# Kernel tuning notes

Hardware: AMD Instinct MI355X
Metric: run time of the kernel (lower is better)

The kernel has to match this reference:

```python
import jax, jax.numpy as jnp
import numpy as np

G = 8          # grid_size
N = G * G      # 64 nodes
DEG = 17       # neighbors per node for 8x8 sudoku (2x4 boxes)
STEPS = 32
H = 96         # hidden_dim
E = 16         # embed_size
B = 16         # batch


def sudoku_edges():
    # row (7) + col (7) + 2x4 box (7) neighbors, set-union -> 17 per node
    idx = np.arange(N).reshape(G, G)
    nb = []
    for j in range(N):
        r, c = j // G, j % G
        br, bc = (r // 2) * 2, (c // 4) * 4
        s = set(idx[r, :].tolist()) | set(idx[:, c].tolist()) | set(idx[br:br + 2, bc:bc + 4].flatten().tolist())
        s.discard(j)
        nb.append(sorted(s))
    return np.asarray(nb, dtype=np.int32)  # [64, 17]


def setup_inputs() -> dict:
    key = jax.random.key(0)
    ks = jax.random.split(key, 16)
    sc = 0.05
    inp = {
        "x": jax.random.randint(ks[0], (B, G, G), 0, G + 1),            # given digits, 0 = blank
        "target": jax.random.randint(ks[1], (B, G, G), 0, G) + 1,       # solutions in 1..8
        "edges": jnp.asarray(sudoku_edges()),                            # [64, 17] int32
        "digit_emb": jax.random.normal(ks[2], (G + 1, E), jnp.float32) * sc,
        "row_emb": jax.random.normal(ks[3], (G, E), jnp.float32) * sc,
        "col_emb": jax.random.normal(ks[4], (G, E), jnp.float32) * sc,
        "in0_W": jax.random.normal(ks[5], (3 * E, H), jnp.float32) * sc,
        "in0_b": jnp.zeros((H,), jnp.float32),
        "in_Ws": jax.random.normal(ks[6], (3, H, H), jnp.float32) * sc,
        "in_bs": jnp.zeros((3, H), jnp.float32),
        "msg0_W": jax.random.normal(ks[7], (2 * H, H), jnp.float32) * sc,
        "msg0_b": jnp.zeros((H,), jnp.float32),
        "msg_Ws": jax.random.normal(ks[8], (3, H, H), jnp.float32) * sc,
        "msg_bs": jnp.zeros((3, H), jnp.float32),
        "W_ih": jax.random.normal(ks[9], (2 * H, 4 * H), jnp.float32) * sc,
        "W_hh": jax.random.normal(ks[10], (H, 4 * H), jnp.float32) * sc,
        "b_ih": jnp.zeros((4 * H,), jnp.float32),
        "b_hh": jnp.zeros((4 * H,), jnp.float32),
        "pred_W": jax.random.normal(ks[11], (H, G), jnp.float32) * sc,
        "pred_b": jnp.zeros((G,), jnp.float32),
    }
    return inp


def _mlp(z, W0, b0, Ws, bs):
    # Linear -> ReLU -> Linear -> ReLU -> Linear -> ReLU -> Linear (def_MLP)
    z = jax.nn.relu(z @ W0 + b0)
    z = jax.nn.relu(z @ Ws[0] + bs[0])
    z = jax.nn.relu(z @ Ws[1] + bs[1])
    return z @ Ws[2] + bs[2]


def reference(x, target, edges, digit_emb, row_emb, col_emb,
              in0_W, in0_b, in_Ws, in_bs,
              msg0_W, msg0_b, msg_Ws, msg_bs,
              W_ih, W_hh, b_ih, b_hh, pred_W, pred_b):
    bsz = x.shape[0]
    xf = x.reshape(bsz, N)
    tgt = target.reshape(bsz, N) - 1                      # labels 0..7

    de = digit_emb[xf]                                    # [B,64,E]
    re = row_emb[jnp.repeat(jnp.arange(G), G)]            # [64,E]
    ce = col_emb[jnp.tile(jnp.arange(G), G)]              # [64,E]
    feat = jnp.concatenate([de,
                            jnp.broadcast_to(re[None], (bsz, N, E)),
                            jnp.broadcast_to(ce[None], (bsz, N, E))], axis=-1)
    xin = _mlp(feat, in0_W, in0_b, in_Ws, in_bs)          # [B,64,H]

    h0 = jnp.zeros((bsz, N, H), jnp.float32)
    s0 = jnp.zeros((bsz * N, H), jnp.float32)

    def step(carry, _):
        h, s, loss = carry
        # gather-by-edge message passing
        h_edges = h[:, edges]                                             # [B,64,17,H]
        h_self = jnp.broadcast_to(h[:, :, None, :], (bsz, N, DEG, H))
        msg = _mlp(jnp.concatenate([h_edges, h_self], -1),
                   msg0_W, msg0_b, msg_Ws, msg_bs).sum(axis=2)            # [B,64,H]
        # LSTMCell update
        lstm_in = jnp.concatenate([msg, xin], -1).reshape(bsz * N, 2 * H)
        gates = lstm_in @ W_ih + b_ih + h.reshape(bsz * N, H) @ W_hh + b_hh
        i, f, g, o = jnp.split(gates, 4, axis=-1)
        s2 = jax.nn.sigmoid(f) * s + jax.nn.sigmoid(i) * jnp.tanh(g)
        h2 = (jax.nn.sigmoid(o) * jnp.tanh(s2)).reshape(bsz, N, H)
        # per-step prediction / loss / accuracy
        logp = jax.nn.log_softmax(h2 @ pred_W + pred_b, axis=-1)          # [B,64,8]
        pred = jnp.argmax(logp, axis=-1)
        acc = jnp.mean(jnp.all(pred == tgt, axis=1).astype(jnp.float32))
        loss_n = -jnp.sum(jnp.take_along_axis(logp, tgt[..., None], -1)) / (bsz * N)
        return (h2, s2, loss + loss_n), acc

    (h, s, loss), accs = jax.lax.scan(step, (h0, s0, jnp.float32(0.0)), None, length=STEPS)
    loss = loss / STEPS
    final_pred = jnp.argmax(h @ pred_W + pred_b, axis=-1)                 # [B,64]
    return loss, accs, final_pred
```

## Files before the change

kernel.cpp:

```cpp
#include <hip/hip_runtime.h>

#define DEG 17
#define NSTEPS 32
#define HD 96
#define NODES 1024

#define WS_U0     0
#define WS_BAR    196608
#define WS_U1     196864
#define WS_XIN    393472
#define WS_GX     491776
#define WS_LOSSP  884992
#define WS_CNTP   893184

#define Z1    0
#define Z2    7680
#define P3    0
#define PL    0
#define PU    0
#define W1L   15360
#define W2L   24576
#define GXL   33792
#define GATES 35328
#define MSGH  36864
#define S3T   37632
#define H2T   38016
#define SLC   38400
#define MSGB  38784
#define M0B   39072
#define LGT   39168
#define NBRI  39200
#define SMTOT 39280

__global__ void init_kernel(
    const int* __restrict__ x,
    const float* __restrict__ digit_emb,
    const float* __restrict__ row_emb,
    const float* __restrict__ col_emb,
    const float* __restrict__ in0_W,
    const float* __restrict__ in0_b,
    const float* __restrict__ in_Ws,
    const float* __restrict__ in_bs,
    const float* __restrict__ msg0_b,
    float* __restrict__ xin,
    float* __restrict__ u0)
{
  const int node = blockIdx.x;
  const int j = threadIdx.x;
  const int n = node & 63;
  const int r = n >> 3, c = n & 7;
  __shared__ float feat[48];
  __shared__ float za[HD];
  __shared__ float zb[HD];
  if (j < 16)      feat[j] = digit_emb[x[node]*16 + j];
  else if (j < 32) feat[j] = row_emb[r*16 + (j-16)];
  else if (j < 48) feat[j] = col_emb[c*16 + (j-32)];
  u0[node*192 + 96 + j] = msg0_b[j];
  __syncthreads();
  float a = in0_b[j];
  for (int k = 0; k < 48; ++k) a = fmaf(feat[k], in0_W[k*HD + j], a);
  za[j] = fmaxf(a, 0.f);
  __syncthreads();
  a = in_bs[j];
  for (int k = 0; k < HD; ++k) a = fmaf(za[k], in_Ws[k*HD + j], a);
  zb[j] = fmaxf(a, 0.f);
  __syncthreads();
  a = in_bs[HD + j];
  for (int k = 0; k < HD; ++k) a = fmaf(zb[k], in_Ws[9216 + k*HD + j], a);
  za[j] = fmaxf(a, 0.f);
  __syncthreads();
  a = in_bs[2*HD + j];
  for (int k = 0; k < HD; ++k) a = fmaf(za[k], in_Ws[2*9216 + k*HD + j], a);
  xin[node*HD + j] = a;
}

__global__ __launch_bounds__(384) void gx_kernel(
    const float* __restrict__ xin, const float* __restrict__ W_ih,
    const float* __restrict__ b_ih, const float* __restrict__ b_hh,
    float* __restrict__ gx)
{
  __shared__ float xs[4*HD];
  const int tid = threadIdx.x;
  const int base = blockIdx.x * 4;
  {
    const int m = tid / HD, k = tid - m*HD;
    xs[m*HD + k] = xin[(base+m)*HD + k];
  }
  __syncthreads();
  const int j = tid;
  float a0 = b_ih[j] + b_hh[j], a1 = a0, a2 = a0, a3 = a0;
  for (int k = 0; k < HD; ++k) {
    const float w = W_ih[(96+k)*384 + j];
    a0 = fmaf(xs[k], w, a0);
    a1 = fmaf(xs[HD+k], w, a1);
    a2 = fmaf(xs[2*HD+k], w, a2);
    a3 = fmaf(xs[3*HD+k], w, a3);
  }
  gx[(base+0)*384 + j] = a0;
  gx[(base+1)*384 + j] = a1;
  gx[(base+2)*384 + j] = a2;
  gx[(base+3)*384 + j] = a3;
}

__global__ __launch_bounds__(512, 1) void solve_kernel(
    const int* __restrict__ edges,
    const float* __restrict__ msg0_W, const float* __restrict__ msg0_b,
    const float* __restrict__ msg_Ws, const float* __restrict__ msg_bs,
    const float* __restrict__ W_ih, const float* __restrict__ W_hh,
    const float* __restrict__ pred_W, const float* __restrict__ pred_b,
    const int* __restrict__ target,
    const float* __restrict__ gx,
    float* __restrict__ u0, float* __restrict__ u1,
    int* bar,
    float* __restrict__ lossP, int* __restrict__ cntP,
    float* __restrict__ final_pred_out)
{
  __shared__ float sm[SMTOT];

  const int tid = threadIdx.x;
  const int blk = blockIdx.x;
  const int bb = blk & 15;
  const int grp = blk >> 4;
  const int nbase = grp * 4;
  const int base = bb*64 + nbase;

  for (int i = tid*4; i < 9216; i += 2048) {
    *(float4*)&sm[W1L + i] = *(const float4*)&msg_Ws[i];
    *(float4*)&sm[W2L + i] = *(const float4*)&msg_Ws[9216 + i];
  }
  #pragma unroll
  for (int t = 0; t < 3; ++t) {
    const int idx = t*512 + tid;
    sm[GXL + idx] = gx[base*384 + idx];
  }
  if (tid < 288) sm[MSGB + tid] = msg_bs[tid];
  if (tid < 96)  sm[M0B + tid]  = msg0_b[tid];
  if (tid < 80) {
    const int m = tid / 20, r = tid % 20;
    ((int*)&sm[NBRI])[tid] = (r < DEG) ? (bb*64 + edges[(nbase+m)*DEG + r])*192 : -1;
  }
  if (tid < 384) {
    sm[SLC + tid] = 0.f;
    sm[MSGH + 384 + tid] = 0.f;
  }
  __syncthreads();

  const float* uP = u0;
  float*       uN = u1;

  for (int st = 0; st < NSTEPS; ++st) {
    if (tid < 480) {
      const int row = tid % 80;
      const int kh  = tid / 80;
      const int m = row / 20;
      const int k0 = kh * 16;
      const int nb = ((const int*)&sm[NBRI])[row];
      if (nb >= 0) {
        const float* ue = uP + nb + k0;
        const float* us = uP + (base+m)*192 + 96 + k0;
        #pragma unroll
        for (int t = 0; t < 4; ++t) {
          const float4 a = *(const float4*)(ue + 4*t);
          const float4 b = *(const float4*)(us + 4*t);
          sm[Z1 + (k0+4*t+0)*80 + row] = fmaxf(a.x + b.x, 0.f);
          sm[Z1 + (k0+4*t+1)*80 + row] = fmaxf(a.y + b.y, 0.f);
          sm[Z1 + (k0+4*t+2)*80 + row] = fmaxf(a.z + b.z, 0.f);
          sm[Z1 + (k0+4*t+3)*80 + row] = fmaxf(a.w + b.w, 0.f);
        }
      } else {
        #pragma unroll
        for (int t = 0; t < 16; ++t) sm[Z1 + (k0+t)*80 + row] = 0.f;
      }
    } else {
      const int i = tid - 480;
      #pragma unroll
      for (int t = 0; t < 12; ++t) sm[S3T + t*32 + i] = 0.f;
    }
    __syncthreads();

    if (tid < 480) {
      const int jg = tid % 24, dg = tid / 24;
      const int j4 = jg*4, d4 = dg*4;
      float acc[4][4] = {{0.f}};
      #pragma unroll 4
      for (int k = 0; k < 96; ++k) {
        const float4 z = *(const float4*)&sm[Z1 + k*80 + d4];
        const float4 w = *(const float4*)&sm[W1L + k*96 + j4];
        const float ze[4] = {z.x, z.y, z.z, z.w};
        const float we[4] = {w.x, w.y, w.z, w.w};
        #pragma unroll
        for (int dd = 0; dd < 4; ++dd)
          #pragma unroll
          for (int jj = 0; jj < 4; ++jj)
            acc[dd][jj] = fmaf(ze[dd], we[jj], acc[dd][jj]);
      }
      #pragma unroll
      for (int jj = 0; jj < 4; ++jj) {
        const float b1 = sm[MSGB + j4 + jj];
        float4 q;
        q.x = fmaxf(acc[0][jj] + b1, 0.f);
        q.y = fmaxf(acc[1][jj] + b1, 0.f);
        q.z = fmaxf(acc[2][jj] + b1, 0.f);
        q.w = fmaxf(acc[3][jj] + b1, 0.f);
        *(float4*)&sm[Z2 + (j4+jj)*80 + d4] = q;
      }
    }
    __syncthreads();

    if (tid < 480) {
      const int jg = tid % 24, dg = tid / 24;
      const int j4 = jg*4, d4 = dg*4;
      float acc[4][4] = {{0.f}};
      #pragma unroll 4
      for (int k = 0; k < 96; ++k) {
        const float4 z = *(const float4*)&sm[Z2 + k*80 + d4];
        const float4 w = *(const float4*)&sm[W2L + k*96 + j4];
        const float ze[4] = {z.x, z.y, z.z, z.w};
        const float we[4] = {w.x, w.y, w.z, w.w};
        #pragma unroll
        for (int dd = 0; dd < 4; ++dd)
          #pragma unroll
          for (int jj = 0; jj < 4; ++jj)
            acc[dd][jj] = fmaf(ze[dd], we[jj], acc[dd][jj]);
      }
      const int nd = d4 / 20;
      const int r0 = d4 - nd*20;
      #pragma unroll
      for (int jj = 0; jj < 4; ++jj) {
        const float b2 = sm[MSGB + 96 + j4 + jj];
        float p = 0.f;
        #pragma unroll
        for (int dd = 0; dd < 4; ++dd)
          if (r0 + dd < DEG) p += fmaxf(acc[dd][jj] + b2, 0.f);
        atomicAdd(&sm[S3T + (j4+jj)*4 + nd], p);
      }
    }
    __syncthreads();

    if (tid < 384) {
      const int jg = tid % 24, kq = tid / 24;
      const int j4 = jg*4, k0 = kq*6;
      const float* W3 = msg_Ws + 2*9216;
      float acc[4][4] = {{0.f}};
      #pragma unroll
      for (int kk = 0; kk < 6; ++kk) {
        const int k = k0 + kk;
        const float4 sv = *(const float4*)&sm[S3T + k*4];
        const float4 wv = *(const float4*)&W3[k*96 + j4];
        const float se[4] = {sv.x, sv.y, sv.z, sv.w};
        const float we[4] = {wv.x, wv.y, wv.z, wv.w};
        #pragma unroll
        for (int m = 0; m < 4; ++m)
          #pragma unroll
          for (int jj = 0; jj < 4; ++jj)
            acc[m][jj] = fmaf(se[m], we[jj], acc[m][jj]);
      }
      #pragma unroll
      for (int m = 0; m < 4; ++m) {
        float4 q = {acc[m][0], acc[m][1], acc[m][2], acc[m][3]};
        *(float4*)&sm[P3 + (kq*4 + m)*96 + j4] = q;
      }
    }
    __syncthreads();
    if (tid < 384) {
      const int m = tid / 96, j = tid % 96;
      float v = 17.f * sm[MSGB + 192 + j];
      #pragma unroll
      for (int kq = 0; kq < 16; ++kq) v += sm[P3 + (kq*4 + m)*96 + j];
      sm[MSGH + j*4 + m] = v;
    }
    __syncthreads();

    {
      const int jg = tid & 63, kq = tid >> 6;
      const int j6 = jg*6, k0 = kq*24;
      const float* Wb = (k0 < 96) ? (W_ih + (size_t)k0*384) : (W_hh + (size_t)(k0-96)*384);
      float acc[4][6] = {{0.f}};
      #pragma unroll 4
      for (int kk = 0; kk < 24; ++kk) {
        const float4 iv = *(const float4*)&sm[MSGH + (k0+kk)*4];
        const float* wp = Wb + kk*384 + j6;
        const float2 wa = *(const float2*)wp;
        const float2 wb2 = *(const float2*)(wp + 2);
        const float2 wc = *(const float2*)(wp + 4);
        const float ie[4] = {iv.x, iv.y, iv.z, iv.w};
        const float we[6] = {wa.x, wa.y, wb2.x, wb2.y, wc.x, wc.y};
        #pragma unroll
        for (int m = 0; m < 4; ++m)
          #pragma unroll
          for (int jj = 0; jj < 6; ++jj)
            acc[m][jj] = fmaf(ie[m], we[jj], acc[m][jj]);
      }
      #pragma unroll
      for (int m = 0; m < 4; ++m) {
        float2 qa = {acc[m][0], acc[m][1]};
        float2 qb = {acc[m][2], acc[m][3]};
        float2 qc = {acc[m][4], acc[m][5]};
        *(float2*)&sm[PL + (kq*4 + m)*384 + j6]     = qa;
        *(float2*)&sm[PL + (kq*4 + m)*384 + j6 + 2] = qb;
        *(float2*)&sm[PL + (kq*4 + m)*384 + j6 + 4] = qc;
      }
    }
    __syncthreads();
    {
      #pragma unroll
      for (int t = 0; t < 3; ++t) {
        const int idx = t*512 + tid;
        const int m = idx / 384, j = idx - m*384;
        float gv = sm[GXL + idx];
        #pragma unroll
        for (int kq = 0; kq < 8; ++kq) gv += sm[PL + (kq*4 + m)*384 + j];
        sm[GATES + idx] = gv;
      }
    }
    __syncthreads();

    if (tid < 384) {
      const int m = tid / 96, hj = tid - m*96;
      const float gi = sm[GATES + m*384 + hj];
      const float gf = sm[GATES + m*384 + 96 + hj];
      const float gg = sm[GATES + m*384 + 192 + hj];
      const float go = sm[GATES + m*384 + 288 + hj];
      const float sv = sm[SLC + tid];
      const float ig = 1.f/(1.f + expf(-gi));
      const float fg = 1.f/(1.f + expf(-gf));
      const float cg = tanhf(gg);
      const float og = 1.f/(1.f + expf(-go));
      const float s2 = fg*sv + ig*cg;
      const float h2 = og*tanhf(s2);
      sm[SLC + tid] = s2;
      sm[H2T + hj*4 + m] = h2;
      sm[MSGH + (96+hj)*4 + m] = h2;
    }
    __syncthreads();

    {
      const int jg = tid & 31, kq = tid >> 5;
      const int j6 = jg*6, k0 = kq*6;
      const float* Wb = (j6 < 96) ? (msg0_W + j6) : (msg0_W + 9216 + j6 - 96);
      float acc[4][6] = {{0.f}};
      #pragma unroll
      for (int kk = 0; kk < 6; ++kk) {
        const int k = k0 + kk;
        const float4 iv = *(const float4*)&sm[H2T + k*4];
        const float* wp = Wb + k*96;
        const float2 wa = *(const float2*)wp;
        const float2 wb2 = *(const float2*)(wp + 2);
        const float2 wc = *(const float2*)(wp + 4);
        const float ie[4] = {iv.x, iv.y, iv.z, iv.w};
        const float we[6] = {wa.x, wa.y, wb2.x, wb2.y, wc.x, wc.y};
        #pragma unroll
        for (int m = 0; m < 4; ++m)
          #pragma unroll
          for (int jj = 0; jj < 6; ++jj)
            acc[m][jj] = fmaf(ie[m], we[jj], acc[m][jj]);
      }
      #pragma unroll
      for (int m = 0; m < 4; ++m) {
        float2 qa = {acc[m][0], acc[m][1]};
        float2 qb = {acc[m][2], acc[m][3]};
        float2 qc = {acc[m][4], acc[m][5]};
        *(float2*)&sm[PU + (kq*4 + m)*192 + j6]     = qa;
        *(float2*)&sm[PU + (kq*4 + m)*192 + j6 + 2] = qb;
        *(float2*)&sm[PU + (kq*4 + m)*192 + j6 + 4] = qc;
      }
    }
    __syncthreads();
    {
      #pragma unroll
      for (int t = 0; t < 2; ++t) {
        const int idx = t*512 + tid;
        if (idx < 768) {
          const int m = idx / 192, j = idx - m*192;
          float v = (j >= 96) ? sm[M0B + j - 96] : 0.f;
          #pragma unroll
          for (int kq = 0; kq < 16; ++kq) v += sm[PU + (kq*4 + m)*192 + j];
          uN[(base+m)*192 + j] = v;
        }
      }
      if (tid >= 384) {
        const int t2 = tid - 384;
        const int m = t2 >> 5, c = (t2 >> 2) & 7, kq2 = t2 & 3;
        float p = 0.f;
        #pragma unroll
        for (int kk = 0; kk < 24; ++kk) {
          const int k = kq2*24 + kk;
          p = fmaf(sm[H2T + k*4 + m], pred_W[k*8 + c], p);
        }
        p += __shfl_xor(p, 1);
        p += __shfl_xor(p, 2);
        if (kq2 == 0) sm[LGT + m*8 + c] = p + pred_b[c];
      }
    }
    __syncthreads();

    if (tid < 4) {
      const int m = tid;
      const int node = base + m;
      float mx = sm[LGT + m*8];
      int pred = 0;
      #pragma unroll
      for (int c = 1; c < 8; ++c) {
        const float v = sm[LGT + m*8 + c];
        if (v > mx) { mx = v; pred = c; }
      }
      float sum = 0.f;
      #pragma unroll
      for (int c = 0; c < 8; ++c) sum += expf(sm[LGT + m*8 + c] - mx);
      const float lse = mx + logf(sum);
      const int tgt = target[node] - 1;
      sm[LGT + 16 + m] = lse - sm[LGT + m*8 + tgt];
      sm[LGT + 20 + m] = (pred == tgt) ? 1.f : 0.f;
      if (st == NSTEPS-1) final_pred_out[node] = (float)pred;
      if (m == 0) {
        lossP[st*256 + blk] = sm[LGT+16] + sm[LGT+17] + sm[LGT+18] + sm[LGT+19];
        cntP[st*256 + blk] = (int)(sm[LGT+20] + sm[LGT+21] + sm[LGT+22] + sm[LGT+23]);
      }
    }

    if (st < NSTEPS-1) {
      __syncthreads();
      if (tid == 0) {
        __hip_atomic_fetch_add(&bar[bb*16], 1, __ATOMIC_RELEASE, __HIP_MEMORY_SCOPE_AGENT);
        const int want = 16*(st+1);
        while (__hip_atomic_load(&bar[bb*16], __ATOMIC_RELAXED, __HIP_MEMORY_SCOPE_AGENT) < want)
          __builtin_amdgcn_s_sleep(2);
        __threadfence();
      }
      __syncthreads();
      float* tp = (float*)uP; uP = uN; uN = tp;
    }
  }
}

__global__ void finalize_kernel(const float* __restrict__ lossP,
                                const int* __restrict__ cntP,
                                float* __restrict__ out)
{
  __shared__ float sl[32];
  const int tid = threadIdx.x;
  const int st = tid >> 3, q = tid & 7;
  float lsum = 0.f;
  for (int i = 0; i < 32; ++i) lsum += lossP[st*256 + q*32 + i];
  lsum += __shfl_xor(lsum, 1);
  lsum += __shfl_xor(lsum, 2);
  lsum += __shfl_xor(lsum, 4);
  if (q == 0) sl[st] = lsum;
  float okc = 0.f;
  #pragma unroll
  for (int t = 0; t < 2; ++t) {
    const int bbat = q + 8*t;
    int c = 0;
    for (int i = 0; i < 16; ++i) c += cntP[st*256 + i*16 + bbat];
    okc += (c == 64) ? 1.f : 0.f;
  }
  okc += __shfl_xor(okc, 1);
  okc += __shfl_xor(okc, 2);
  okc += __shfl_xor(okc, 4);
  if (q == 0) out[1 + st] = okc / 16.f;
  __syncthreads();
  if (tid == 0) {
    float tot = 0.f;
    for (int i = 0; i < 32; ++i) tot += sl[i];
    out[0] = tot / ((float)NODES * (float)NSTEPS);
  }
}

extern "C" void kernel_launch(void* const* d_in, const int* in_sizes, int n_in,
                              void* d_out, int out_size, void* d_ws, size_t ws_size,
                              hipStream_t stream) {
  const int*   x         = (const int*)  d_in[0];
  const int*   target    = (const int*)  d_in[1];
  const int*   edges     = (const int*)  d_in[2];
  const float* digit_emb = (const float*)d_in[3];
  const float* row_emb   = (const float*)d_in[4];
  const float* col_emb   = (const float*)d_in[5];
  const float* in0_W     = (const float*)d_in[6];
  const float* in0_b     = (const float*)d_in[7];
  const float* in_Ws     = (const float*)d_in[8];
  const float* in_bs     = (const float*)d_in[9];
  const float* msg0_W    = (const float*)d_in[10];
  const float* msg0_b    = (const float*)d_in[11];
  const float* msg_Ws    = (const float*)d_in[12];
  const float* msg_bs    = (const float*)d_in[13];
  const float* W_ih      = (const float*)d_in[14];
  const float* W_hh      = (const float*)d_in[15];
  const float* b_ih      = (const float*)d_in[16];
  const float* b_hh      = (const float*)d_in[17];
  const float* pred_W    = (const float*)d_in[18];
  const float* pred_b    = (const float*)d_in[19];

  float* ws    = (float*)d_ws;
  float* u0    = ws + WS_U0;
  int*   bar   = (int*)(ws + WS_BAR);
  float* u1    = ws + WS_U1;
  float* xin   = ws + WS_XIN;
  float* gxb   = ws + WS_GX;
  float* lossP = ws + WS_LOSSP;
  int*   cntP  = (int*)(ws + WS_CNTP);

  hipMemsetAsync(d_ws, 0, (size_t)(196608 + 256)*sizeof(float), stream);

  init_kernel<<<NODES, HD, 0, stream>>>(x, digit_emb, row_emb, col_emb,
                                        in0_W, in0_b, in_Ws, in_bs,
                                        msg0_b, xin, u0);
  gx_kernel<<<256, 384, 0, stream>>>(xin, W_ih, b_ih, b_hh, gxb);

  float* outp = (float*)d_out;
  solve_kernel<<<256, 512, 0, stream>>>(
      edges, msg0_W, msg0_b, msg_Ws, msg_bs,
      W_ih, W_hh, pred_W, pred_b, target, gxb,
      u0, u1, bar, lossP, cntP, outp + 1 + NSTEPS);

  finalize_kernel<<<1, 256, 0, stream>>>(lossP, cntP, outp);
}
```

Baseline: 1.097 ms.

## Split each block into two independent 256-thread halves with per-half LDS barriers

Each 512-thread block now runs as two 256-thread halves, each owning 2 of the block's 4 nodes with its own shared-memory workspace. The block-wide __syncthreads between stages are replaced by a counter-based barrier in LDS, so one half can move ahead without waiting for the other. The aim is to cut synchronisation stalls and let the two halves overlap their phases; in exchange the spin-wait barrier adds overhead, and each half still loads the shared weights. The partial loss and count arrays are re-indexed to 512 entries per step to match.

```diff
diff --git a/kernel.cpp b/kernel.cpp
--- a/kernel.cpp
+++ b/kernel.cpp
@@ -3,7 +3,6 @@
 #define DEG 17
 #define NSTEPS 32
 #define HD 96
-#define NODES 1024
 
 #define WS_U0     0
 #define WS_BAR    196608
@@ -11,26 +10,26 @@
 #define WS_XIN    393472
 #define WS_GX     491776
 #define WS_LOSSP  884992
-#define WS_CNTP   893184
-
-#define Z1    0
-#define Z2    7680
-#define P3    0
-#define PL    0
-#define PU    0
-#define W1L   15360
-#define W2L   24576
-#define GXL   33792
-#define GATES 35328
-#define MSGH  36864
-#define S3T   37632
-#define H2T   38016
-#define SLC   38400
-#define MSGB  38784
-#define M0B   39072
-#define LGT   39168
-#define NBRI  39200
-#define SMTOT 39280
+#define WS_CNTP   901376
+
+#define W1L   0
+#define W2L   9216
+#define MSGB  18432
+#define M0B   18720
+#define VBASE 18816
+#define VSTR  10272
+#define VZ1    0
+#define VZ2    3840
+#define VGX    7680
+#define VGATES 8448
+#define VMSGH  9216
+#define VS3T   9600
+#define VH2T   9792
+#define VSLC   9984
+#define VLGT   10176
+#define VNBRI  10208
+#define BARC  (VBASE + 2*VSTR)
+#define SMTOT (BARC + 8)
 
 __global__ void init_kernel(
     const int* __restrict__ x,
@@ -102,6 +101,13 @@
   gx[(base+3)*384 + j] = a3;
 }
 
+__device__ __forceinline__ void vbar(int* c, int want) {
+  if ((threadIdx.x & 63) == 0)
+    __hip_atomic_fetch_add(c, 1, __ATOMIC_RELEASE, __HIP_MEMORY_SCOPE_WORKGROUP);
+  while (__hip_atomic_load(c, __ATOMIC_ACQUIRE, __HIP_MEMORY_SCOPE_WORKGROUP) < want)
+    __builtin_amdgcn_s_sleep(1);
+}
+
 __global__ __launch_bounds__(512, 1) void solve_kernel(
     const int* __restrict__ edges,
     const float* __restrict__ msg0_W, const float* __restrict__ msg0_b,
@@ -118,73 +124,81 @@
   __shared__ float sm[SMTOT];
 
   const int tid = threadIdx.x;
+  const int vb  = tid >> 8;
+  const int vt  = tid & 255;
   const int blk = blockIdx.x;
-  const int bb = blk & 15;
+  const int bb  = blk & 15;
   const int grp = blk >> 4;
-  const int nbase = grp * 4;
-  const int base = bb*64 + nbase;
+  const int base = bb*64 + grp*4;
+  const int gbase = base + vb*2;
+
+  float* const vs = sm + VBASE + vb*VSTR;
+  int* const vnbri = (int*)(vs + VNBRI);
+  int* const vbc = (int*)(sm + BARC) + vb;
 
   for (int i = tid*4; i < 9216; i += 2048) {
     *(float4*)&sm[W1L + i] = *(const float4*)&msg_Ws[i];
     *(float4*)&sm[W2L + i] = *(const float4*)&msg_Ws[9216 + i];
   }
+  if (tid < 288) sm[MSGB + tid] = msg_bs[tid];
+  if (tid < 96)  sm[M0B + tid]  = msg0_b[tid];
+  if (tid < 2)   ((int*)(sm + BARC))[tid] = 0;
   #pragma unroll
   for (int t = 0; t < 3; ++t) {
-    const int idx = t*512 + tid;
-    sm[GXL + idx] = gx[base*384 + idx];
-  }
-  if (tid < 288) sm[MSGB + tid] = msg_bs[tid];
-  if (tid < 96)  sm[M0B + tid]  = msg0_b[tid];
-  if (tid < 80) {
-    const int m = tid / 20, r = tid % 20;
-    ((int*)&sm[NBRI])[tid] = (r < DEG) ? (bb*64 + edges[(nbase+m)*DEG + r])*192 : -1;
-  }
-  if (tid < 384) {
-    sm[SLC + tid] = 0.f;
-    sm[MSGH + 384 + tid] = 0.f;
+    const int idx = t*256 + vt;
+    vs[VGX + idx] = gx[gbase*384 + idx];
+  }
+  if (vt < 192) {
+    vs[VSLC + vt] = 0.f;
+    vs[VMSGH + 192 + vt] = 0.f;
+  }
+  if (vt < 40) {
+    const int m = vt / 20, r = vt % 20;
+    vnbri[vt] = (r < DEG) ? (bb*64 + edges[((grp*4 + vb*2) + m)*DEG + r])*192 : -1;
   }
   __syncthreads();
 
   const float* uP = u0;
   float*       uN = u1;
+  int vph = 0;
 
   for (int st = 0; st < NSTEPS; ++st) {
-    if (tid < 480) {
-      const int row = tid % 80;
-      const int kh  = tid / 80;
+    if (vt < 240) {
+      const int row = vt % 40;
+      const int kh  = vt / 40;
       const int m = row / 20;
       const int k0 = kh * 16;
-      const int nb = ((const int*)&sm[NBRI])[row];
+      const int nb = vnbri[row];
       if (nb >= 0) {
         const float* ue = uP + nb + k0;
-        const float* us = uP + (base+m)*192 + 96 + k0;
+        const float* us = uP + (gbase+m)*192 + 96 + k0;
         #pragma unroll
         for (int t = 0; t < 4; ++t) {
           const float4 a = *(const float4*)(ue + 4*t);
           const float4 b = *(const float4*)(us + 4*t);
-          sm[Z1 + (k0+4*t+0)*80 + row] = fmaxf(a.x + b.x, 0.f);
-          sm[Z1 + (k0+4*t+1)*80 + row] = fmaxf(a.y + b.y, 0.f);
-          sm[Z1 + (k0+4*t+2)*80 + row] = fmaxf(a.z + b.z, 0.f);
-          sm[Z1 + (k0+4*t+3)*80 + row] = fmaxf(a.w + b.w, 0.f);
+          vs[VZ1 + (k0+4*t+0)*40 + row] = fmaxf(a.x + b.x, 0.f);
+          vs[VZ1 + (k0+4*t+1)*40 + row] = fmaxf(a.y + b.y, 0.f);
+          vs[VZ1 + (k0+4*t+2)*40 + row] = fmaxf(a.z + b.z, 0.f);
+          vs[VZ1 + (k0+4*t+3)*40 + row] = fmaxf(a.w + b.w, 0.f);
         }
       } else {
         #pragma unroll
-        for (int t = 0; t < 16; ++t) sm[Z1 + (k0+t)*80 + row] = 0.f;
+        for (int t = 0; t < 16; ++t) vs[VZ1 + (k0+t)*40 + row] = 0.f;
       }
     } else {
-      const int i = tid - 480;
-      #pragma unroll
-      for (int t = 0; t < 12; ++t) sm[S3T + t*32 + i] = 0.f;
-    }
-    __syncthreads();
-
-    if (tid < 480) {
-      const int jg = tid % 24, dg = tid / 24;
+      const int i = vt - 240;
+      #pragma unroll
+      for (int t = 0; t < 12; ++t) vs[VS3T + i*12 + t] = 0.f;
+    }
+    vph += 4; vbar(vbc, vph);
+
+    if (vt < 240) {
+      const int jg = vt % 24, dg = vt / 24;
       const int j4 = jg*4, d4 = dg*4;
       float acc[4][4] = {{0.f}};
       #pragma unroll 4
       for (int k = 0; k < 96; ++k) {
-        const float4 z = *(const float4*)&sm[Z1 + k*80 + d4];
+        const float4 z = *(const float4*)&vs[VZ1 + k*40 + d4];
         const float4 w = *(const float4*)&sm[W1L + k*96 + j4];
         const float ze[4] = {z.x, z.y, z.z, z.w};
         const float we[4] = {w.x, w.y, w.z, w.w};
@@ -202,18 +216,18 @@
         q.y = fmaxf(acc[1][jj] + b1, 0.f);
         q.z = fmaxf(acc[2][jj] + b1, 0.f);
         q.w = fmaxf(acc[3][jj] + b1, 0.f);
-        *(float4*)&sm[Z2 + (j4+jj)*80 + d4] = q;
-      }
-    }
-    __syncthreads();
-
-    if (tid < 480) {
-      const int jg = tid % 24, dg = tid / 24;
+        *(float4*)&vs[VZ2 + (j4+jj)*40 + d4] = q;
+      }
+    }
+    vph += 4; vbar(vbc, vph);
+
+    if (vt < 240) {
+      const int jg = vt % 24, dg = vt / 24;
       const int j4 = jg*4, d4 = dg*4;
       float acc[4][4] = {{0.f}};
       #pragma unroll 4
       for (int k = 0; k < 96; ++k) {
-        const float4 z = *(const float4*)&sm[Z2 + k*80 + d4];
+        const float4 z = *(const float4*)&vs[VZ2 + k*40 + d4];
         const float4 w = *(const float4*)&sm[W2L + k*96 + j4];
         const float ze[4] = {z.x, z.y, z.z, z.w};
         const float we[4] = {w.x, w.y, w.z, w.w};
@@ -232,189 +246,186 @@
         #pragma unroll
         for (int dd = 0; dd < 4; ++dd)
           if (r0 + dd < DEG) p += fmaxf(acc[dd][jj] + b2, 0.f);
-        atomicAdd(&sm[S3T + (j4+jj)*4 + nd], p);
-      }
-    }
-    __syncthreads();
-
-    if (tid < 384) {
-      const int jg = tid % 24, kq = tid / 24;
-      const int j4 = jg*4, k0 = kq*6;
+        atomicAdd(&vs[VS3T + (j4+jj)*2 + nd], p);
+      }
+    }
+    vph += 4; vbar(vbc, vph);
+
+    if (vt < 192) {
+      const int jg = vt % 24, kq = vt / 24;
+      const int j4 = jg*4, k0 = kq*12;
       const float* W3 = msg_Ws + 2*9216;
-      float acc[4][4] = {{0.f}};
-      #pragma unroll
-      for (int kk = 0; kk < 6; ++kk) {
+      float acc[2][4] = {{0.f}};
+      #pragma unroll
+      for (int kk = 0; kk < 12; ++kk) {
         const int k = k0 + kk;
-        const float4 sv = *(const float4*)&sm[S3T + k*4];
+        const float2 sv = *(const float2*)&vs[VS3T + k*2];
         const float4 wv = *(const float4*)&W3[k*96 + j4];
-        const float se[4] = {sv.x, sv.y, sv.z, sv.w};
+        const float se[2] = {sv.x, sv.y};
         const float we[4] = {wv.x, wv.y, wv.z, wv.w};
         #pragma unroll
-        for (int m = 0; m < 4; ++m)
+        for (int m = 0; m < 2; ++m)
           #pragma unroll
           for (int jj = 0; jj < 4; ++jj)
             acc[m][jj] = fmaf(se[m], we[jj], acc[m][jj]);
       }
       #pragma unroll
-      for (int m = 0; m < 4; ++m) {
+      for (int m = 0; m < 2; ++m) {
         float4 q = {acc[m][0], acc[m][1], acc[m][2], acc[m][3]};
-        *(float4*)&sm[P3 + (kq*4 + m)*96 + j4] = q;
-      }
-    }
-    __syncthreads();
-    if (tid < 384) {
-      const int m = tid / 96, j = tid % 96;
+        *(float4*)&vs[VZ1 + (kq*2 + m)*96 + j4] = q;
+      }
+    }
+    vph += 4; vbar(vbc, vph);
+    if (vt < 192) {
+      const int m = vt / 96, j = vt % 96;
       float v = 17.f * sm[MSGB + 192 + j];
       #pragma unroll
-      for (int kq = 0; kq < 16; ++kq) v += sm[P3 + (kq*4 + m)*96 + j];
-      sm[MSGH + j*4 + m] = v;
-    }
-    __syncthreads();
+      for (int kq = 0; kq < 8; ++kq) v += vs[VZ1 + (kq*2 + m)*96 + j];
+      vs[VMSGH + j*2 + m] = v;
+    }
+    vph += 4; vbar(vbc, vph);
 
     {
-      const int jg = tid & 63, kq = tid >> 6;
-      const int j6 = jg*6, k0 = kq*24;
+      const int jg = vt & 63, kq = vt >> 6;
+      const int j6 = jg*6, k0 = kq*48;
       const float* Wb = (k0 < 96) ? (W_ih + (size_t)k0*384) : (W_hh + (size_t)(k0-96)*384);
-      float acc[4][6] = {{0.f}};
+      float acc[2][6] = {{0.f}};
       #pragma unroll 4
-      for (int kk = 0; kk < 24; ++kk) {
-        const float4 iv = *(const float4*)&sm[MSGH + (k0+kk)*4];
+      for (int kk = 0; kk < 48; ++kk) {
+        const float2 iv = *(const float2*)&vs[VMSGH + (k0+kk)*2];
         const float* wp = Wb + kk*384 + j6;
         const float2 wa = *(const float2*)wp;
         const float2 wb2 = *(const float2*)(wp + 2);
         const float2 wc = *(const float2*)(wp + 4);
-        const float ie[4] = {iv.x, iv.y, iv.z, iv.w};
+        const float ie[2] = {iv.x, iv.y};
         const float we[6] = {wa.x, wa.y, wb2.x, wb2.y, wc.x, wc.y};
         #pragma unroll
-        for (int m = 0; m < 4; ++m)
+        for (int m = 0; m < 2; ++m)
           #pragma unroll
           for (int jj = 0; jj < 6; ++jj)
             acc[m][jj] = fmaf(ie[m], we[jj], acc[m][jj]);
       }
       #pragma unroll
-      for (int m = 0; m < 4; ++m) {
+      for (int m = 0; m < 2; ++m) {
         float2 qa = {acc[m][0], acc[m][1]};
         float2 qb = {acc[m][2], acc[m][3]};
         float2 qc = {acc[m][4], acc[m][5]};
-        *(float2*)&sm[PL + (kq*4 + m)*384 + j6]     = qa;
-        *(float2*)&sm[PL + (kq*4 + m)*384 + j6 + 2] = qb;
-        *(float2*)&sm[PL + (kq*4 + m)*384 + j6 + 4] = qc;
-      }
-    }
-    __syncthreads();
+        *(float2*)&vs[VZ1 + (kq*2 + m)*384 + j6]     = qa;
+        *(float2*)&vs[VZ1 + (kq*2 + m)*384 + j6 + 2] = qb;
+        *(float2*)&vs[VZ1 + (kq*2 + m)*384 + j6 + 4] = qc;
+      }
+    }
+    vph += 4; vbar(vbc, vph);
     {
       #pragma unroll
       for (int t = 0; t < 3; ++t) {
-        const int idx = t*512 + tid;
+        const int idx = t*256 + vt;
         const int m = idx / 384, j = idx - m*384;
-        float gv = sm[GXL + idx];
-        #pragma unroll
-        for (int kq = 0; kq < 8; ++kq) gv += sm[PL + (kq*4 + m)*384 + j];
-        sm[GATES + idx] = gv;
-      }
-    }
-    __syncthreads();
-
-    if (tid < 384) {
-      const int m = tid / 96, hj = tid - m*96;
-      const float gi = sm[GATES + m*384 + hj];
-      const float gf = sm[GATES + m*384 + 96 + hj];
-      const float gg = sm[GATES + m*384 + 192 + hj];
-      const float go = sm[GATES + m*384 + 288 + hj];
-      const float sv = sm[SLC + tid];
+        float gv = vs[VGX + idx];
+        #pragma unroll
+        for (int kq = 0; kq < 4; ++kq) gv += vs[VZ1 + (kq*2 + m)*384 + j];
+        vs[VGATES + idx] = gv;
+      }
+    }
+    vph += 4; vbar(vbc, vph);
+
+    if (vt < 192) {
+      const int m = vt / 96, hj = vt - m*96;
+      const float gi = vs[VGATES + m*384 + hj];
+      const float gf = vs[VGATES + m*384 + 96 + hj];
+      const float gg = vs[VGATES + m*384 + 192 + hj];
+      const float go = vs[VGATES + m*384 + 288 + hj];
+      const float sv = vs[VSLC + vt];
       const float ig = 1.f/(1.f + expf(-gi));
       const float fg = 1.f/(1.f + expf(-gf));
       const float cg = tanhf(gg);
       const float og = 1.f/(1.f + expf(-go));
       const float s2 = fg*sv + ig*cg;
       const float h2 = og*tanhf(s2);
-      sm[SLC + tid] = s2;
-      sm[H2T + hj*4 + m] = h2;
-      sm[MSGH + (96+hj)*4 + m] = h2;
-    }
-    __syncthreads();
+      vs[VSLC + vt] = s2;
+      vs[VH2T + hj*2 + m] = h2;
+      vs[VMSGH + (96+hj)*2 + m] = h2;
+    }
+    vph += 4; vbar(vbc, vph);
 
     {
-      const int jg = tid & 31, kq = tid >> 5;
-      const int j6 = jg*6, k0 = kq*6;
+      const int jg = vt & 31, kq = vt >> 5;
+      const int j6 = jg*6, k0 = kq*12;
       const float* Wb = (j6 < 96) ? (msg0_W + j6) : (msg0_W + 9216 + j6 - 96);
-      float acc[4][6] = {{0.f}};
-      #pragma unroll
-      for (int kk = 0; kk < 6; ++kk) {
+      float acc[2][6] = {{0.f}};
+      #pragma unroll
+      for (int kk = 0; kk < 12; ++kk) {
         const int k = k0 + kk;
-        const float4 iv = *(const float4*)&sm[H2T + k*4];
+        const float2 iv = *(const float2*)&vs[VH2T + k*2];
         const float* wp = Wb + k*96;
         const float2 wa = *(const float2*)wp;
         const float2 wb2 = *(const float2*)(wp + 2);
         const float2 wc = *(const float2*)(wp + 4);
-        const float ie[4] = {iv.x, iv.y, iv.z, iv.w};
+        const float ie[2] = {iv.x, iv.y};
         const float we[6] = {wa.x, wa.y, wb2.x, wb2.y, wc.x, wc.y};
         #pragma unroll
-        for (int m = 0; m < 4; ++m)
+        for (int m = 0; m < 2; ++m)
           #pragma unroll
           for (int jj = 0; jj < 6; ++jj)
             acc[m][jj] = fmaf(ie[m], we[jj], acc[m][jj]);
       }
       #pragma unroll
-      for (int m = 0; m < 4; ++m) {
+      for (int m = 0; m < 2; ++m) {
         float2 qa = {acc[m][0], acc[m][1]};
         float2 qb = {acc[m][2], acc[m][3]};
         float2 qc = {acc[m][4], acc[m][5]};
-        *(float2*)&sm[PU + (kq*4 + m)*192 + j6]     = qa;
-        *(float2*)&sm[PU + (kq*4 + m)*192 + j6 + 2] = qb;
-        *(float2*)&sm[PU + (kq*4 + m)*192 + j6 + 4] = qc;
-      }
-    }
-    __syncthreads();
-    {
+        *(float2*)&vs[VZ1 + (kq*2 + m)*192 + j6]     = qa;
+        *(float2*)&vs[VZ1 + (kq*2 + m)*192 + j6 + 2] = qb;
+        *(float2*)&vs[VZ1 + (kq*2 + m)*192 + j6 + 4] = qc;
+      }
+    }
+    vph += 4; vbar(vbc, vph);
+    if (vt < 192) {
       #pragma unroll
       for (int t = 0; t < 2; ++t) {
-        const int idx = t*512 + tid;
-        if (idx < 768) {
-          const int m = idx / 192, j = idx - m*192;
-          float v = (j >= 96) ? sm[M0B + j - 96] : 0.f;
-          #pragma unroll
-          for (int kq = 0; kq < 16; ++kq) v += sm[PU + (kq*4 + m)*192 + j];
-          uN[(base+m)*192 + j] = v;
-        }
-      }
-      if (tid >= 384) {
-        const int t2 = tid - 384;
-        const int m = t2 >> 5, c = (t2 >> 2) & 7, kq2 = t2 & 3;
-        float p = 0.f;
-        #pragma unroll
-        for (int kk = 0; kk < 24; ++kk) {
-          const int k = kq2*24 + kk;
-          p = fmaf(sm[H2T + k*4 + m], pred_W[k*8 + c], p);
-        }
-        p += __shfl_xor(p, 1);
-        p += __shfl_xor(p, 2);
-        if (kq2 == 0) sm[LGT + m*8 + c] = p + pred_b[c];
-      }
-    }
-    __syncthreads();
-
-    if (tid < 4) {
-      const int m = tid;
-      const int node = base + m;
-      float mx = sm[LGT + m*8];
+        const int idx = t*192 + vt;
+        const int m = idx / 192, j = idx - m*192;
+        float v = (j >= 96) ? sm[M0B + j - 96] : 0.f;
+        #pragma unroll
+        for (int kq = 0; kq < 8; ++kq) v += vs[VZ1 + (kq*2 + m)*192 + j];
+        uN[(gbase+m)*192 + j] = v;
+      }
+    } else {
+      const int t2 = vt - 192;
+      const int m = t2 >> 5, c = (t2 >> 2) & 7, kq2 = t2 & 3;
+      float p = 0.f;
+      #pragma unroll
+      for (int kk = 0; kk < 24; ++kk) {
+        const int k = kq2*24 + kk;
+        p = fmaf(vs[VH2T + k*2 + m], pred_W[k*8 + c], p);
+      }
+      p += __shfl_xor(p, 1);
+      p += __shfl_xor(p, 2);
+      if (kq2 == 0) vs[VLGT + m*8 + c] = p + pred_b[c];
+    }
+    vph += 4; vbar(vbc, vph);
+
+    if (vt < 2) {
+      const int m = vt;
+      const int node = gbase + m;
+      float mx = vs[VLGT + m*8];
       int pred = 0;
       #pragma unroll
       for (int c = 1; c < 8; ++c) {
-        const float v = sm[LGT + m*8 + c];
+        const float v = vs[VLGT + m*8 + c];
         if (v > mx) { mx = v; pred = c; }
       }
       float sum = 0.f;
       #pragma unroll
-      for (int c = 0; c < 8; ++c) sum += expf(sm[LGT + m*8 + c] - mx);
+      for (int c = 0; c < 8; ++c) sum += expf(vs[VLGT + m*8 + c] - mx);
       const float lse = mx + logf(sum);
       const int tgt = target[node] - 1;
-      sm[LGT + 16 + m] = lse - sm[LGT + m*8 + tgt];
-      sm[LGT + 20 + m] = (pred == tgt) ? 1.f : 0.f;
+      vs[VLGT + 16 + m] = lse - vs[VLGT + m*8 + tgt];
+      vs[VLGT + 20 + m] = (pred == tgt) ? 1.f : 0.f;
       if (st == NSTEPS-1) final_pred_out[node] = (float)pred;
       if (m == 0) {
-        lossP[st*256 + blk] = sm[LGT+16] + sm[LGT+17] + sm[LGT+18] + sm[LGT+19];
-        cntP[st*256 + blk] = (int)(sm[LGT+20] + sm[LGT+21] + sm[LGT+22] + sm[LGT+23]);
+        lossP[st*512 + bb*32 + grp*2 + vb] = vs[VLGT+16] + vs[VLGT+17];
+        cntP[st*512 + bb*32 + grp*2 + vb] = (int)(vs[VLGT+20] + vs[VLGT+21]);
       }
     }
 
@@ -441,7 +452,7 @@
   const int tid = threadIdx.x;
   const int st = tid >> 3, q = tid & 7;
   float lsum = 0.f;
-  for (int i = 0; i < 32; ++i) lsum += lossP[st*256 + q*32 + i];
+  for (int i = 0; i < 64; ++i) lsum += lossP[st*512 + q*64 + i];
   lsum += __shfl_xor(lsum, 1);
   lsum += __shfl_xor(lsum, 2);
   lsum += __shfl_xor(lsum, 4);
@@ -451,7 +462,7 @@
   for (int t = 0; t < 2; ++t) {
     const int bbat = q + 8*t;
     int c = 0;
-    for (int i = 0; i < 16; ++i) c += cntP[st*256 + i*16 + bbat];
+    for (int i = 0; i < 32; ++i) c += cntP[st*512 + bbat*32 + i];
     okc += (c == 64) ? 1.f : 0.f;
   }
   okc += __shfl_xor(okc, 1);
@@ -462,7 +473,7 @@
   if (tid == 0) {
     float tot = 0.f;
     for (int i = 0; i < 32; ++i) tot += sl[i];
-    out[0] = tot / ((float)NODES * (float)NSTEPS);
+    out[0] = tot / (1024.f * (float)NSTEPS);
   }
 }
 
@@ -501,9 +512,9 @@
 
   hipMemsetAsync(d_ws, 0, (size_t)(196608 + 256)*sizeof(float), stream);
 
-  init_kernel<<<NODES, HD, 0, stream>>>(x, digit_emb, row_emb, col_emb,
-                                        in0_W, in0_b, in_Ws, in_bs,
-                                        msg0_b, xin, u0);
+  init_kernel<<<1024, HD, 0, stream>>>(x, digit_emb, row_emb, col_emb,
+                                       in0_W, in0_b, in_Ws, in_bs,
+                                       msg0_b, xin, u0);
   gx_kernel<<<256, 384, 0, stream>>>(xin, W_ih, b_ih, b_hh, gxb);
 
   float* outp = (float*)d_out;
```

Result: faster. 1.034 ms (-5.8%).
